# Performance work log

Measured on AMD Instinct MI355X. Metric: run time of the kernel, lower is better.

## Reference

```python
import jax, jax.numpy as jnp
import numpy as np

HOP = jnp.array([0, 1, 4, 7, 2, 5, 8, 3, 6, 9, 11, 14, 10, 12, 15, 13, 16])
GRAPH = jnp.array([0, 1, 4, 7, 2, 5, 8, 3, 6, 9, 12, 10, 13, 15, 11, 14, 16])
D_MODEL, L, D_INNER, D_STATE, DT_RANK = 512, 17, 1024, 4, 32


def layernorm(x, w, b, eps=1e-5):
    mu = x.mean(-1, keepdims=True)
    var = ((x - mu) ** 2).mean(-1, keepdims=True)
    return (x - mu) * jax.lax.rsqrt(var + eps) * w + b


def setup_inputs() -> dict:
    key = jax.random.key(0)
    ks = jax.random.split(key, 9)
    B = 4096
    s = lambda k, shape: jax.random.normal(k, shape, jnp.float32) * 0.02
    # A_log init per mamba_ssm: log(1..d_state) repeated over d_inner
    A_log = jnp.log(jnp.broadcast_to(jnp.arange(1, D_STATE + 1, dtype=jnp.float32), (D_INNER, D_STATE)))
    return {
        "x": jax.random.normal(ks[0], (B, L, D_MODEL), jnp.float32),
        "bp_embed": s(ks[1], (1, 5, D_MODEL)),
        "ln_w": jnp.ones((D_MODEL,), jnp.float32),
        "ln_b": jnp.zeros((D_MODEL,), jnp.float32),
        "in_proj_w": s(ks[2], (2 * D_INNER, D_MODEL)),
        "conv_w": 1.0 + s(ks[3], (D_INNER,)),  # d_conv=1 depthwise conv == per-channel scale
        "conv_b": jnp.zeros((D_INNER,), jnp.float32),
        "x_proj_w": s(ks[4], (DT_RANK + 2 * D_STATE, D_INNER)),
        "dt_proj_w": s(ks[5], (D_INNER, DT_RANK)),
        "dt_proj_b": s(ks[6], (D_INNER,)) - 4.0,  # softplus-inverse-ish small dt init
        "A_log": A_log,
        "D": jnp.ones((D_INNER,), jnp.float32),
        "out_proj_w": s(ks[7], (D_MODEL, D_INNER)),
    }


def mamba(u, in_proj_w, conv_w, conv_b, x_proj_w, dt_proj_w, dt_proj_b, A_log, D, out_proj_w):
    # u: [B, L, d_model]
    xz = jnp.einsum('bld,ed->ble', u, in_proj_w)          # [B,L,2*d_inner]
    xm, z = jnp.split(xz, 2, axis=-1)
    xm = jax.nn.silu(xm * conv_w + conv_b)                 # d_conv=1 -> pointwise
    x_dbl = jnp.einsum('ble,fe->blf', xm, x_proj_w)        # [B,L,dt_rank+2*d_state]
    dt_r = x_dbl[..., :DT_RANK]
    Bm = x_dbl[..., DT_RANK:DT_RANK + D_STATE]
    Cm = x_dbl[..., DT_RANK + D_STATE:]
    dt = jax.nn.softplus(jnp.einsum('blr,er->ble', dt_r, dt_proj_w) + dt_proj_b)  # [B,L,d_inner]
    A = -jnp.exp(A_log)                                    # [d_inner,d_state]

    def step(h, inp):
        dt_t, B_t, C_t, x_t = inp                          # [B,di],[B,ds],[B,ds],[B,di]
        dA = jnp.exp(dt_t[..., None] * A)                  # [B,di,ds]
        h = dA * h + (dt_t * x_t)[..., None] * B_t[:, None, :]
        y = jnp.einsum('bes,bs->be', h, C_t)
        return h, y

    bsz = u.shape[0]
    h0 = jnp.zeros((bsz, D_INNER, D_STATE), u.dtype)
    seq = (dt.transpose(1, 0, 2), Bm.transpose(1, 0, 2), Cm.transpose(1, 0, 2), xm.transpose(1, 0, 2))
    _, ys = jax.lax.scan(step, h0, seq)                    # ys: [L,B,d_inner]
    y = ys.transpose(1, 0, 2) + xm * D
    y = y * jax.nn.silu(z)
    return jnp.einsum('ble,de->bld', y, out_proj_w)


def reference(x, bp_embed, ln_w, ln_b, in_proj_w, conv_w, conv_b, x_proj_w,
              dt_proj_w, dt_proj_b, A_log, D, out_proj_w):
    bp = bp_embed
    x_bpe = jnp.concatenate([bp[:, :3], bp[:, :3], bp[:, :3], bp[:, :1],
                             bp[:, 3:], bp[:, :1], bp[:, 3:], bp[:, 3:]], axis=1)  # [1,17,dim]
    x_ssm = x[:, HOP, :] + x_bpe
    x_ssm = layernorm(x_ssm, ln_w, ln_b)
    x_ssm = mamba(x_ssm, in_proj_w, conv_w, conv_b, x_proj_w,
                  dt_proj_w, dt_proj_b, A_log, D, out_proj_w)
    return x + x_ssm[:, GRAPH, :]
```

## Files before the change

kernel.cpp:

```cpp
#include <hip/hip_runtime.h>

typedef unsigned short u16;
typedef unsigned int   u32;
typedef __bf16 bf16_t;
typedef bf16_t bf16x8 __attribute__((ext_vector_type(8)));
typedef float  f32x4  __attribute__((ext_vector_type(4)));

#define DEV static __device__ __forceinline__

__constant__ int c_HOP[17] = {0,1,4,7,2,5,8,3,6,9,11,14,10,12,15,13,16};
__constant__ int c_BPE[17] = {0,1,2,0,1,2,0,1,2,0,3,4,0,3,4,3,4};

DEV u16 f2bf(float f){
  u32 x = __builtin_bit_cast(u32, f);
  x += 0x7fffu + ((x >> 16) & 1u);
  return (u16)(x >> 16);
}
DEV float bf2f(u32 u){ return __builtin_bit_cast(float, u << 16); }
DEV float silu_f(float v){ return v / (1.f + __expf(-v)); }
DEV float softplus_f(float s){ return (s > 20.f) ? s : log1pf(__expf(s)); }

DEV void gll16(const void* g, void* l){
  __builtin_amdgcn_global_load_lds((__attribute__((address_space(1))) void*)g,
                                   (__attribute__((address_space(3))) void*)l,
                                   16, 0, 0);
}

__global__ __launch_bounds__(256) void cvt4(
    const float* __restrict__ s0, u16* __restrict__ d0, int n0,
    const float* __restrict__ s1, u16* __restrict__ d1, int n1,
    const float* __restrict__ s2, u16* __restrict__ d2, int n2,
    const float* __restrict__ s3, u16* __restrict__ d3, int n3)
{
  int t = blockIdx.x * 256 + threadIdx.x;
  if (t < n0){ d0[t] = f2bf(s0[t]); return; }
  t -= n0; if (t < n1){ d1[t] = f2bf(s1[t]); return; }
  t -= n1; if (t < n2){ d2[t] = f2bf(s2[t]); return; }
  t -= n2; if (t < n3){ d3[t] = f2bf(s3[t]); }
}

__global__ __launch_bounds__(256) void ln_gather(
    const float* __restrict__ x, const float* __restrict__ bpe,
    const float* __restrict__ lnw, const float* __restrict__ lnb,
    u16* __restrict__ u)
{
  int tok = blockIdx.x;
  int b = tok / 17;
  int l = tok - b * 17;
  const float* xr = x   + ((size_t)b * 17 + c_HOP[l]) * 512;
  const float* br = bpe + (size_t)c_BPE[l] * 512;
  int tid = threadIdx.x;
  int d0 = tid * 2;
  float2 xv = *(const float2*)(xr + d0);
  float2 bv = *(const float2*)(br + d0);
  float v0 = xv.x + bv.x, v1 = xv.y + bv.y;

  __shared__ float red[8];
  float s = v0 + v1;
  #pragma unroll
  for (int o = 32; o; o >>= 1) s += __shfl_xor(s, o);
  if ((tid & 63) == 0) red[tid >> 6] = s;
  __syncthreads();
  float mu = (red[0] + red[1] + red[2] + red[3]) * (1.f / 512.f);
  float a0 = v0 - mu, a1 = v1 - mu;
  float q = a0 * a0 + a1 * a1;
  #pragma unroll
  for (int o = 32; o; o >>= 1) q += __shfl_xor(q, o);
  if ((tid & 63) == 0) red[4 + (tid >> 6)] = q;
  __syncthreads();
  float var = (red[4] + red[5] + red[6] + red[7]) * (1.f / 512.f);
  float rs = rsqrtf(var + 1e-5f);

  u16 o0 = f2bf(a0 * rs * lnw[d0]     + lnb[d0]);
  u16 o1 = f2bf(a1 * rs * lnw[d0 + 1] + lnb[d0 + 1]);
  u32 pack = (u32)o0 | ((u32)o1 << 16);
  *(u32*)(u + (size_t)tok * 512 + d0) = pack;
}

enum { EPI_SPLIT = 0, EPI_OUT = 1 };

template<int EPI>
__global__ __launch_bounds__(512, 2) void gemm256(
    const u16* __restrict__ A, int lda,
    const u16* __restrict__ W, int K, int MT,
    u16* __restrict__ ob0, u16* __restrict__ ob1,
    const float* __restrict__ p0, const float* __restrict__ p1,
    const float* __restrict__ xres, float* __restrict__ fout)
{
  __shared__ u16 smem[65536];

  int nwg = gridDim.x;
  int cpx = nwg >> 3;
  int wg = (blockIdx.x & 7) * cpx + (blockIdx.x >> 3);
  int NT = nwg / MT;
  int nt = wg % NT, mt = wg / NT;
  int brow = mt * 256, bcol = nt * 256;
  int tid = threadIdx.x, lane = tid & 63, wid = tid >> 6;
  int wm = wid >> 2, wn = wid & 3;
  int l15 = lane & 15, lhi = lane >> 4;

  f32x4 acc[8][4] = {};

  int sr0 = tid >> 2, sr1 = 128 + (tid >> 2), sch = tid & 3;
  const u16* gA0 = A + (size_t)(brow + sr0) * lda + (sch ^ ((sr0 >> 1) & 3)) * 8;
  const u16* gA1 = A + (size_t)(brow + sr1) * lda + (sch ^ ((sr1 >> 1) & 3)) * 8;
  const u16* gW0 = W + (size_t)(bcol + sr0) * K   + (sch ^ ((sr0 >> 1) & 3)) * 8;
  const u16* gW1 = W + (size_t)(bcol + sr1) * K   + (sch ^ ((sr1 >> 1) & 3)) * 8;

  auto stA = [&](int buf, int kh, int koff) {
    char* d = (char*)smem + (buf * 2 + kh) * 16384 + tid * 16;
    gll16(gA0 + koff, d);
    gll16(gA1 + koff, d + 8192);
  };
  auto stB = [&](int buf, int kh, int koff) {
    char* d = (char*)smem + 65536 + (buf * 2 + kh) * 16384 + tid * 16;
    gll16(gW0 + koff, d);
    gll16(gW1 + koff, d + 8192);
  };

  int aoff[2][4], boff[4];
  #pragma unroll
  for (int mh = 0; mh < 2; mh++)
    #pragma unroll
    for (int mi = 0; mi < 4; mi++) {
      int r = wm * 128 + mh * 64 + mi * 16 + l15;
      aoff[mh][mi] = r * 64 + ((lhi ^ ((r >> 1) & 3)) * 16);
    }
  #pragma unroll
  for (int ni = 0; ni < 4; ni++) {
    int r = wn * 64 + ni * 16 + l15;
    boff[ni] = r * 64 + ((lhi ^ ((r >> 1) & 3)) * 16);
  }

#define HALF(BUF, KH)                                                        \
  {                                                                          \
    const char* la = (const char*)smem + ((BUF) * 2 + (KH)) * 16384;         \
    const char* lb = (const char*)smem + 65536 + ((BUF) * 2 + (KH)) * 16384; \
    bf16x8 bv0 = *(const bf16x8*)(lb + boff[0]);                             \
    bf16x8 bv1 = *(const bf16x8*)(lb + boff[1]);                             \
    bf16x8 bv2 = *(const bf16x8*)(lb + boff[2]);                             \
    bf16x8 bv3 = *(const bf16x8*)(lb + boff[3]);                             \
    bf16x8 a0 = *(const bf16x8*)(la + aoff[0][0]);                           \
    bf16x8 a1 = *(const bf16x8*)(la + aoff[0][1]);                           \
    bf16x8 a2 = *(const bf16x8*)(la + aoff[0][2]);                           \
    bf16x8 a3 = *(const bf16x8*)(la + aoff[0][3]);                           \
    __builtin_amdgcn_s_setprio(1);                                           \
    acc[0][0] = __builtin_amdgcn_mfma_f32_16x16x32_bf16(a0, bv0, acc[0][0],0,0,0); \
    acc[1][0] = __builtin_amdgcn_mfma_f32_16x16x32_bf16(a1, bv0, acc[1][0],0,0,0); \
    acc[2][0] = __builtin_amdgcn_mfma_f32_16x16x32_bf16(a2, bv0, acc[2][0],0,0,0); \
    acc[3][0] = __builtin_amdgcn_mfma_f32_16x16x32_bf16(a3, bv0, acc[3][0],0,0,0); \
    acc[0][1] = __builtin_amdgcn_mfma_f32_16x16x32_bf16(a0, bv1, acc[0][1],0,0,0); \
    acc[1][1] = __builtin_amdgcn_mfma_f32_16x16x32_bf16(a1, bv1, acc[1][1],0,0,0); \
    acc[2][1] = __builtin_amdgcn_mfma_f32_16x16x32_bf16(a2, bv1, acc[2][1],0,0,0); \
    acc[3][1] = __builtin_amdgcn_mfma_f32_16x16x32_bf16(a3, bv1, acc[3][1],0,0,0); \
    acc[0][2] = __builtin_amdgcn_mfma_f32_16x16x32_bf16(a0, bv2, acc[0][2],0,0,0); \
    acc[1][2] = __builtin_amdgcn_mfma_f32_16x16x32_bf16(a1, bv2, acc[1][2],0,0,0); \
    acc[2][2] = __builtin_amdgcn_mfma_f32_16x16x32_bf16(a2, bv2, acc[2][2],0,0,0); \
    acc[3][2] = __builtin_amdgcn_mfma_f32_16x16x32_bf16(a3, bv2, acc[3][2],0,0,0); \
    acc[0][3] = __builtin_amdgcn_mfma_f32_16x16x32_bf16(a0, bv3, acc[0][3],0,0,0); \
    acc[1][3] = __builtin_amdgcn_mfma_f32_16x16x32_bf16(a1, bv3, acc[1][3],0,0,0); \
    acc[2][3] = __builtin_amdgcn_mfma_f32_16x16x32_bf16(a2, bv3, acc[2][3],0,0,0); \
    acc[3][3] = __builtin_amdgcn_mfma_f32_16x16x32_bf16(a3, bv3, acc[3][3],0,0,0); \
    a0 = *(const bf16x8*)(la + aoff[1][0]);                                  \
    a1 = *(const bf16x8*)(la + aoff[1][1]);                                  \
    a2 = *(const bf16x8*)(la + aoff[1][2]);                                  \
    a3 = *(const bf16x8*)(la + aoff[1][3]);                                  \
    acc[4][0] = __builtin_amdgcn_mfma_f32_16x16x32_bf16(a0, bv0, acc[4][0],0,0,0); \
    acc[5][0] = __builtin_amdgcn_mfma_f32_16x16x32_bf16(a1, bv0, acc[5][0],0,0,0); \
    acc[6][0] = __builtin_amdgcn_mfma_f32_16x16x32_bf16(a2, bv0, acc[6][0],0,0,0); \
    acc[7][0] = __builtin_amdgcn_mfma_f32_16x16x32_bf16(a3, bv0, acc[7][0],0,0,0); \
    acc[4][1] = __builtin_amdgcn_mfma_f32_16x16x32_bf16(a0, bv1, acc[4][1],0,0,0); \
    acc[5][1] = __builtin_amdgcn_mfma_f32_16x16x32_bf16(a1, bv1, acc[5][1],0,0,0); \
    acc[6][1] = __builtin_amdgcn_mfma_f32_16x16x32_bf16(a2, bv1, acc[6][1],0,0,0); \
    acc[7][1] = __builtin_amdgcn_mfma_f32_16x16x32_bf16(a3, bv1, acc[7][1],0,0,0); \
    acc[4][2] = __builtin_amdgcn_mfma_f32_16x16x32_bf16(a0, bv2, acc[4][2],0,0,0); \
    acc[5][2] = __builtin_amdgcn_mfma_f32_16x16x32_bf16(a1, bv2, acc[5][2],0,0,0); \
    acc[6][2] = __builtin_amdgcn_mfma_f32_16x16x32_bf16(a2, bv2, acc[6][2],0,0,0); \
    acc[7][2] = __builtin_amdgcn_mfma_f32_16x16x32_bf16(a3, bv2, acc[7][2],0,0,0); \
    acc[4][3] = __builtin_amdgcn_mfma_f32_16x16x32_bf16(a0, bv3, acc[4][3],0,0,0); \
    acc[5][3] = __builtin_amdgcn_mfma_f32_16x16x32_bf16(a1, bv3, acc[5][3],0,0,0); \
    acc[6][3] = __builtin_amdgcn_mfma_f32_16x16x32_bf16(a2, bv3, acc[6][3],0,0,0); \
    acc[7][3] = __builtin_amdgcn_mfma_f32_16x16x32_bf16(a3, bv3, acc[7][3],0,0,0); \
    __builtin_amdgcn_s_setprio(0);                                           \
  }

  int T = K >> 6;

  stA(0, 0, 0);  stB(0, 0, 0);
  stA(0, 1, 32); stB(0, 1, 32);
  stA(1, 0, 64); stB(1, 0, 64);
  asm volatile("s_waitcnt vmcnt(8)" ::: "memory");
  __builtin_amdgcn_s_barrier();
  __builtin_amdgcn_sched_barrier(0);

  for (int t = 0; t < T; ++t) {
    int bb_ = t & 1;
    if (t + 1 < T) { int ko = ((t + 1) << 6) + 32; stA(bb_ ^ 1, 1, ko); stB(bb_ ^ 1, 1, ko); }
    HALF(bb_, 0);
    if (t < T - 1) { asm volatile("s_waitcnt vmcnt(8)" ::: "memory"); }
    else           { asm volatile("s_waitcnt vmcnt(0)" ::: "memory"); }
    __builtin_amdgcn_s_barrier();
    __builtin_amdgcn_sched_barrier(0);
    if (t + 2 < T) { int ko = (t + 2) << 6; stA(bb_, 0, ko); stB(bb_, 0, ko); }
    HALF(bb_, 1);
    if (t < T - 2)      { asm volatile("s_waitcnt vmcnt(8)" ::: "memory"); }
    else if (t == T - 2){ asm volatile("s_waitcnt vmcnt(4)" ::: "memory"); }
    else                { asm volatile("s_waitcnt vmcnt(0)" ::: "memory"); }
    __builtin_amdgcn_s_barrier();
    __builtin_amdgcn_sched_barrier(0);
  }
#undef HALF

  if constexpr (EPI == EPI_SPLIT) {
    u16* cl = smem;
    bool isx = (bcol < 1024);
    #pragma unroll
    for (int fm = 0; fm < 8; fm++) {
      int lrow = wm * 128 + fm * 16 + lhi * 4;
      #pragma unroll
      for (int ni = 0; ni < 4; ni++) {
        int col = wn * 64 + ni * 16 + l15;
        int cidx = isx ? (bcol + col) : 0;
        float cw = isx ? p0[cidx] : 1.f;
        float cb = isx ? p1[cidx] : 0.f;
        #pragma unroll
        for (int rr = 0; rr < 4; rr++)
          cl[(lrow + rr) * 256 + col] = f2bf(silu_f(acc[fm][ni][rr] * cw + cb));
      }
    }
    __syncthreads();
    int colbase = isx ? bcol : (bcol - 1024);
    u16* dst = isx ? ob0 : ob1;
    #pragma unroll
    for (int i = 0; i < 16; i++) {
      int idx = i * 512 + tid;
      int row = idx >> 5;
      int q = idx & 31;
      uint4 v = *(const uint4*)(cl + row * 256 + q * 8);
      *(uint4*)(dst + (size_t)(brow + row) * 1024 + colbase + q * 8) = v;
    }
  } else {
    float* cf = (float*)smem;
    #pragma unroll
    for (int mh = 0; mh < 2; mh++) {
      __syncthreads();
      if (wm == mh) {
        #pragma unroll
        for (int fm = 0; fm < 8; fm++) {
          int lrow = fm * 16 + lhi * 4;
          #pragma unroll
          for (int ni = 0; ni < 4; ni++) {
            int col = wn * 64 + ni * 16 + l15;
            #pragma unroll
            for (int rr = 0; rr < 4; rr++)
              cf[(lrow + rr) * 256 + col] = acc[fm][ni][rr];
          }
        }
      }
      __syncthreads();
      #pragma unroll
      for (int i = 0; i < 16; i++) {
        int idx = i * 512 + tid;
        int row = idx >> 6;
        int q = idx & 63;
        int grow = brow + mh * 128 + row;
        u32 bq = (u32)grow / 17u;
        int gl = grow - (int)bq * 17;
        size_t orow = (size_t)bq * 17 + c_HOP[gl];
        size_t off = orow * 512 + bcol + q * 4;
        float4 xv = *(const float4*)(xres + off);
        const float* cp = cf + row * 256 + q * 4;
        float4 ov;
        ov.x = xv.x + cp[0]; ov.y = xv.y + cp[1];
        ov.z = xv.z + cp[2]; ov.w = xv.w + cp[3];
        *(float4*)(fout + off) = ov;
      }
    }
  }
}

enum { EPI_XDBL = 0, EPI_DT = 1 };

template<int EPI>
__global__ __launch_bounds__(256) void gemm_bt(
    const u16* __restrict__ A, int lda,
    const u16* __restrict__ W, int K, int MT,
    u16* __restrict__ ob0, const float* __restrict__ p0)
{
  __shared__ u16 sm[16384];
  int nwg = gridDim.x;
  int cpx = nwg >> 3;
  int wg = (blockIdx.x & 7) * cpx + (blockIdx.x >> 3);
  int NT = nwg / MT;
  int nt = wg % NT, mt = wg / NT;
  int brow = mt * 128, bcol = nt * 128;
  int tid = threadIdx.x, lane = tid & 63, wid = tid >> 6;
  int wm = wid >> 1, wn = wid & 1;

  f32x4 acc[4][4] = {};

  int srow = tid >> 2;
  int sch  = tid & 3;

  const u16* gA0 = A + (size_t)(brow + srow)      * lda + (sch ^ ((srow >> 1) & 3)) * 8;
  const u16* gA1 = A + (size_t)(brow + 64 + srow) * lda + (sch ^ (((64 + srow) >> 1) & 3)) * 8;
  const u16* gW0 = W + (size_t)(bcol + srow)      * K   + (sch ^ ((srow >> 1) & 3)) * 8;
  const u16* gW1 = W + (size_t)(bcol + 64 + srow) * K   + (sch ^ (((64 + srow) >> 1) & 3)) * 8;

  auto STAGE = [&](int buf, int kt) {
    char* dA = (char*)sm + buf * 8192 + tid * 16;
    char* dW = (char*)sm + 16384 + buf * 8192 + tid * 16;
    gll16(gA0 + kt, dA);
    gll16(gA1 + kt, dA + 4096);
    gll16(gW0 + kt, dW);
    gll16(gW1 + kt, dW + 4096);
  };

  int aoff[4], boff[4];
  #pragma unroll
  for (int mi = 0; mi < 4; mi++) {
    int r = wm * 64 + mi * 16 + (lane & 15);
    aoff[mi] = r * 64 + (((lane >> 4) ^ ((r >> 1) & 3)) * 16);
  }
  #pragma unroll
  for (int ni = 0; ni < 4; ni++) {
    int r = wn * 64 + ni * 16 + (lane & 15);
    boff[ni] = r * 64 + (((lane >> 4) ^ ((r >> 1) & 3)) * 16);
  }

  auto COMPUTE = [&](int buf) {
    const char* la = (const char*)sm + buf * 8192;
    const char* lb = (const char*)sm + 16384 + buf * 8192;
    bf16x8 av[4], bv[4];
    #pragma unroll
    for (int mi = 0; mi < 4; mi++)
      av[mi] = *(const bf16x8*)(la + aoff[mi]);
    #pragma unroll
    for (int ni = 0; ni < 4; ni++)
      bv[ni] = *(const bf16x8*)(lb + boff[ni]);
    #pragma unroll
    for (int mi = 0; mi < 4; mi++)
      #pragma unroll
      for (int ni = 0; ni < 4; ni++)
        acc[mi][ni] = __builtin_amdgcn_mfma_f32_16x16x32_bf16(
            av[mi], bv[ni], acc[mi][ni], 0, 0, 0);
  };

  int nsteps = K >> 5;
  STAGE(0, 0);
  __syncthreads();
  int cur = 0;
  for (int s = 1; s < nsteps; ++s) {
    STAGE(cur ^ 1, s << 5);
    COMPUTE(cur);
    __syncthreads();
    cur ^= 1;
  }
  COMPUTE(cur);

  int r4 = (lane >> 4) * 4;
  int cl15 = lane & 15;
  if constexpr (EPI == EPI_XDBL) {
    #pragma unroll
    for (int mi = 0; mi < 4; mi++) {
      int rowb = brow + wm * 64 + mi * 16 + r4;
      #pragma unroll
      for (int ni = 0; ni < 4; ni++) {
        int col = bcol + wn * 64 + ni * 16 + cl15;
        if (col < 40) {
          #pragma unroll
          for (int rr = 0; rr < 4; rr++)
            ob0[(size_t)(rowb + rr) * 40 + col] = f2bf(acc[mi][ni][rr]);
        }
      }
    }
  } else {
    __syncthreads();
    u16* cls = sm;
    #pragma unroll
    for (int mi = 0; mi < 4; mi++) {
      int lrow = wm * 64 + mi * 16 + r4;
      #pragma unroll
      for (int ni = 0; ni < 4; ni++) {
        int lcol = wn * 64 + ni * 16 + cl15;
        float bb = p0[bcol + lcol];
        #pragma unroll
        for (int rr = 0; rr < 4; rr++)
          cls[(lrow + rr) * 128 + lcol] = f2bf(softplus_f(acc[mi][ni][rr] + bb));
      }
    }
    __syncthreads();
    #pragma unroll
    for (int i = 0; i < 8; i++) {
      int idx = i * 256 + tid;
      int row = idx >> 4;
      int q = idx & 15;
      uint4 v = *(const uint4*)(cls + row * 128 + q * 8);
      *(uint4*)(ob0 + (size_t)(brow + row) * 1024 + bcol + q * 8) = v;
    }
  }
}

__global__ __launch_bounds__(128) void scan5(
    const u16* __restrict__ xm, const u16* __restrict__ zs,
    const u16* __restrict__ xdbl, u16* __restrict__ dty,
    const float* __restrict__ A_log, const float* __restrict__ Dp)
{
  int b = blockIdx.x;
  int tid = threadIdx.x;
  int e0 = tid * 8;
  const size_t base = (size_t)b * 17 * 1024;

  float4 al = *(const float4*)(A_log + (size_t)e0 * 4);
  float A0 = -__expf(al.x), A1 = -__expf(al.y);
  float A2 = -__expf(al.z), A3 = -__expf(al.w);
  float Dv[8];
  *(float4*)(Dv)     = *(const float4*)(Dp + e0);
  *(float4*)(Dv + 4) = *(const float4*)(Dp + e0 + 4);

  const u16* xmb = xm + base + e0;
  const u16* zsb = zs + base + e0;
  u16* db = dty + base + e0;
  const u16* bcb = xdbl + (size_t)b * 680 + 32;

  float h[8][4];
  #pragma unroll
  for (int c = 0; c < 8; c++)
    #pragma unroll
    for (int s = 0; s < 4; s++) h[c][s] = 0.f;

  #pragma unroll
  for (int t = 0; t < 17; t++) {
    uint4 xr = *(const uint4*)(xmb + t * 1024);
    uint4 zr = *(const uint4*)(zsb + t * 1024);
    uint4 dr = *(const uint4*)(db + t * 1024);
    uint4 bc = *(const uint4*)(bcb + t * 40);
    float B0 = bf2f(bc.x & 0xffffu), B1 = bf2f(bc.x >> 16);
    float B2 = bf2f(bc.y & 0xffffu), B3 = bf2f(bc.y >> 16);
    float C0 = bf2f(bc.z & 0xffffu), C1 = bf2f(bc.z >> 16);
    float C2 = bf2f(bc.w & 0xffffu), C3 = bf2f(bc.w >> 16);
    u32 yo[4];
    const u32* xw = (const u32*)&xr;
    const u32* zw = (const u32*)&zr;
    const u32* dw = (const u32*)&dr;
    #pragma unroll
    for (int c = 0; c < 8; c++) {
      u32 x16 = (c & 1) ? (xw[c >> 1] >> 16) : (xw[c >> 1] & 0xffffu);
      u32 z16 = (c & 1) ? (zw[c >> 1] >> 16) : (zw[c >> 1] & 0xffffu);
      u32 d16 = (c & 1) ? (dw[c >> 1] >> 16) : (dw[c >> 1] & 0xffffu);
      float xv = bf2f(x16), zv = bf2f(z16), dtv = bf2f(d16);
      float dx = dtv * xv;
      h[c][0] = __expf(dtv * A0) * h[c][0] + dx * B0;
      h[c][1] = __expf(dtv * A1) * h[c][1] + dx * B1;
      h[c][2] = __expf(dtv * A2) * h[c][2] + dx * B2;
      h[c][3] = __expf(dtv * A3) * h[c][3] + dx * B3;
      float yv = h[c][0] * C0 + h[c][1] * C1 + h[c][2] * C2 + h[c][3] * C3;
      u16 pk = f2bf((yv + xv * Dv[c]) * zv);
      if (c & 1) yo[c >> 1] |= ((u32)pk << 16);
      else       yo[c >> 1] = (u32)pk;
    }
    *(uint4*)(db + t * 1024) = *(uint4*)yo;
  }
}

extern "C" void kernel_launch(void* const* d_in, const int* in_sizes, int n_in,
                              void* d_out, int out_size, void* d_ws, size_t ws_size,
                              hipStream_t stream) {
  const float* x     = (const float*)d_in[0];
  const float* bpe   = (const float*)d_in[1];
  const float* lnw   = (const float*)d_in[2];
  const float* lnb   = (const float*)d_in[3];
  const float* w_in  = (const float*)d_in[4];
  const float* convw = (const float*)d_in[5];
  const float* convb = (const float*)d_in[6];
  const float* w_xp  = (const float*)d_in[7];
  const float* w_dt  = (const float*)d_in[8];
  const float* b_dt  = (const float*)d_in[9];
  const float* A_log = (const float*)d_in[10];
  const float* Dp    = (const float*)d_in[11];
  const float* w_out = (const float*)d_in[12];
  float* out = (float*)d_out;

  u16* ws = (u16*)d_ws;
  u16* wb_in  = ws;
  u16* wb_out = wb_in  + 1048576;
  u16* wb_xp  = wb_out + 524288;
  u16* wb_dt  = wb_xp  + 40960;
  u16* xm     = wb_dt  + 32768;
  u16* zs     = xm     + 71303168;
  u16* xdbl   = zs     + 71303168;
  u16* dty    = xdbl   + 2785280;
  u16* u      = dty;

  const int MT2 = 272;
  const int MT1 = 544;

  cvt4<<<6432, 256, 0, stream>>>(w_in, wb_in, 1048576, w_out, wb_out, 524288,
                                 w_xp, wb_xp, 40960, w_dt, wb_dt, 32768);

  ln_gather<<<69632, 256, 0, stream>>>(x, bpe, lnw, lnb, u);

  gemm256<EPI_SPLIT><<<MT2 * 8, 512, 0, stream>>>(
      u, 512, wb_in, 512, MT2, xm, zs, convw, convb, nullptr, nullptr);

  gemm_bt<EPI_XDBL><<<MT1 * 1, 256, 0, stream>>>(
      xm, 1024, wb_xp, 1024, MT1, xdbl, nullptr);

  gemm_bt<EPI_DT><<<MT1 * 8, 256, 0, stream>>>(
      xdbl, 40, wb_dt, 32, MT1, dty, b_dt);

  scan5<<<4096, 128, 0, stream>>>(xm, zs, xdbl, dty, A_log, Dp);

  gemm256<EPI_OUT><<<MT2 * 2, 512, 0, stream>>>(
      dty, 1024, wb_out, 1024, MT2, nullptr, nullptr, nullptr, nullptr, x, out);
}
```

Baseline: 842.3 us.

## Reschedule GEMM main loop into four barrier phases and swizzle epilogue LDS staging

The big GEMM main loop is split into four phases per K-step, each loading A fragments and issuing the next tile's global-to-LDS loads for one operand before a barrier and MFMA cluster. The prefetch depth drops from two half-tiles ahead to one full tile ahead, with a single vmcnt wait every two phases. Separately, the epilogue LDS staging buffers in the fused-GEMM and dt GEMM kernels are written and read with a row-dependent rotated column index to avoid bank conflicts. The extra barriers add synchronisation cost, and the shallower prefetch may expose more global-load latency.

```diff
diff --git a/kernel.cpp b/kernel.cpp
--- a/kernel.cpp
+++ b/kernel.cpp
@@ -132,84 +132,77 @@
     boff[ni] = r * 64 + ((lhi ^ ((r >> 1) & 3)) * 16);
   }
 
-#define HALF(BUF, KH)                                                        \
-  {                                                                          \
-    const char* la = (const char*)smem + ((BUF) * 2 + (KH)) * 16384;         \
-    const char* lb = (const char*)smem + 65536 + ((BUF) * 2 + (KH)) * 16384; \
-    bf16x8 bv0 = *(const bf16x8*)(lb + boff[0]);                             \
-    bf16x8 bv1 = *(const bf16x8*)(lb + boff[1]);                             \
-    bf16x8 bv2 = *(const bf16x8*)(lb + boff[2]);                             \
-    bf16x8 bv3 = *(const bf16x8*)(lb + boff[3]);                             \
-    bf16x8 a0 = *(const bf16x8*)(la + aoff[0][0]);                           \
-    bf16x8 a1 = *(const bf16x8*)(la + aoff[0][1]);                           \
-    bf16x8 a2 = *(const bf16x8*)(la + aoff[0][2]);                           \
-    bf16x8 a3 = *(const bf16x8*)(la + aoff[0][3]);                           \
-    __builtin_amdgcn_s_setprio(1);                                           \
-    acc[0][0] = __builtin_amdgcn_mfma_f32_16x16x32_bf16(a0, bv0, acc[0][0],0,0,0); \
-    acc[1][0] = __builtin_amdgcn_mfma_f32_16x16x32_bf16(a1, bv0, acc[1][0],0,0,0); \
-    acc[2][0] = __builtin_amdgcn_mfma_f32_16x16x32_bf16(a2, bv0, acc[2][0],0,0,0); \
-    acc[3][0] = __builtin_amdgcn_mfma_f32_16x16x32_bf16(a3, bv0, acc[3][0],0,0,0); \
-    acc[0][1] = __builtin_amdgcn_mfma_f32_16x16x32_bf16(a0, bv1, acc[0][1],0,0,0); \
-    acc[1][1] = __builtin_amdgcn_mfma_f32_16x16x32_bf16(a1, bv1, acc[1][1],0,0,0); \
-    acc[2][1] = __builtin_amdgcn_mfma_f32_16x16x32_bf16(a2, bv1, acc[2][1],0,0,0); \
-    acc[3][1] = __builtin_amdgcn_mfma_f32_16x16x32_bf16(a3, bv1, acc[3][1],0,0,0); \
-    acc[0][2] = __builtin_amdgcn_mfma_f32_16x16x32_bf16(a0, bv2, acc[0][2],0,0,0); \
-    acc[1][2] = __builtin_amdgcn_mfma_f32_16x16x32_bf16(a1, bv2, acc[1][2],0,0,0); \
-    acc[2][2] = __builtin_amdgcn_mfma_f32_16x16x32_bf16(a2, bv2, acc[2][2],0,0,0); \
-    acc[3][2] = __builtin_amdgcn_mfma_f32_16x16x32_bf16(a3, bv2, acc[3][2],0,0,0); \
-    acc[0][3] = __builtin_amdgcn_mfma_f32_16x16x32_bf16(a0, bv3, acc[0][3],0,0,0); \
-    acc[1][3] = __builtin_amdgcn_mfma_f32_16x16x32_bf16(a1, bv3, acc[1][3],0,0,0); \
-    acc[2][3] = __builtin_amdgcn_mfma_f32_16x16x32_bf16(a2, bv3, acc[2][3],0,0,0); \
-    acc[3][3] = __builtin_amdgcn_mfma_f32_16x16x32_bf16(a3, bv3, acc[3][3],0,0,0); \
-    a0 = *(const bf16x8*)(la + aoff[1][0]);                                  \
-    a1 = *(const bf16x8*)(la + aoff[1][1]);                                  \
-    a2 = *(const bf16x8*)(la + aoff[1][2]);                                  \
-    a3 = *(const bf16x8*)(la + aoff[1][3]);                                  \
-    acc[4][0] = __builtin_amdgcn_mfma_f32_16x16x32_bf16(a0, bv0, acc[4][0],0,0,0); \
-    acc[5][0] = __builtin_amdgcn_mfma_f32_16x16x32_bf16(a1, bv0, acc[5][0],0,0,0); \
-    acc[6][0] = __builtin_amdgcn_mfma_f32_16x16x32_bf16(a2, bv0, acc[6][0],0,0,0); \
-    acc[7][0] = __builtin_amdgcn_mfma_f32_16x16x32_bf16(a3, bv0, acc[7][0],0,0,0); \
-    acc[4][1] = __builtin_amdgcn_mfma_f32_16x16x32_bf16(a0, bv1, acc[4][1],0,0,0); \
-    acc[5][1] = __builtin_amdgcn_mfma_f32_16x16x32_bf16(a1, bv1, acc[5][1],0,0,0); \
-    acc[6][1] = __builtin_amdgcn_mfma_f32_16x16x32_bf16(a2, bv1, acc[6][1],0,0,0); \
-    acc[7][1] = __builtin_amdgcn_mfma_f32_16x16x32_bf16(a3, bv1, acc[7][1],0,0,0); \
-    acc[4][2] = __builtin_amdgcn_mfma_f32_16x16x32_bf16(a0, bv2, acc[4][2],0,0,0); \
-    acc[5][2] = __builtin_amdgcn_mfma_f32_16x16x32_bf16(a1, bv2, acc[5][2],0,0,0); \
-    acc[6][2] = __builtin_amdgcn_mfma_f32_16x16x32_bf16(a2, bv2, acc[6][2],0,0,0); \
-    acc[7][2] = __builtin_amdgcn_mfma_f32_16x16x32_bf16(a3, bv2, acc[7][2],0,0,0); \
-    acc[4][3] = __builtin_amdgcn_mfma_f32_16x16x32_bf16(a0, bv3, acc[4][3],0,0,0); \
-    acc[5][3] = __builtin_amdgcn_mfma_f32_16x16x32_bf16(a1, bv3, acc[5][3],0,0,0); \
-    acc[6][3] = __builtin_amdgcn_mfma_f32_16x16x32_bf16(a2, bv3, acc[6][3],0,0,0); \
-    acc[7][3] = __builtin_amdgcn_mfma_f32_16x16x32_bf16(a3, bv3, acc[7][3],0,0,0); \
-    __builtin_amdgcn_s_setprio(0);                                           \
+  bf16x8 bvv[4];
+
+#define PH(BUF, KH, MH, LOADB, STMT, WAIT)                                  \
+  {                                                                         \
+    const char* la = (const char*)smem + ((BUF) * 2 + (KH)) * 16384;        \
+    bf16x8 a0 = *(const bf16x8*)(la + aoff[MH][0]);                         \
+    bf16x8 a1 = *(const bf16x8*)(la + aoff[MH][1]);                         \
+    bf16x8 a2 = *(const bf16x8*)(la + aoff[MH][2]);                         \
+    bf16x8 a3 = *(const bf16x8*)(la + aoff[MH][3]);                         \
+    if (LOADB) {                                                            \
+      const char* lb = (const char*)smem + 65536 + ((BUF) * 2 + (KH)) * 16384; \
+      bvv[0] = *(const bf16x8*)(lb + boff[0]);                              \
+      bvv[1] = *(const bf16x8*)(lb + boff[1]);                              \
+      bvv[2] = *(const bf16x8*)(lb + boff[2]);                              \
+      bvv[3] = *(const bf16x8*)(lb + boff[3]);                              \
+    }                                                                       \
+    STMT                                                                    \
+    __builtin_amdgcn_sched_barrier(0);                                      \
+    __builtin_amdgcn_s_barrier();                                           \
+    __builtin_amdgcn_s_setprio(1);                                          \
+    acc[(MH)*4+0][0] = __builtin_amdgcn_mfma_f32_16x16x32_bf16(a0, bvv[0], acc[(MH)*4+0][0],0,0,0); \
+    acc[(MH)*4+1][0] = __builtin_amdgcn_mfma_f32_16x16x32_bf16(a1, bvv[0], acc[(MH)*4+1][0],0,0,0); \
+    acc[(MH)*4+2][0] = __builtin_amdgcn_mfma_f32_16x16x32_bf16(a2, bvv[0], acc[(MH)*4+2][0],0,0,0); \
+    acc[(MH)*4+3][0] = __builtin_amdgcn_mfma_f32_16x16x32_bf16(a3, bvv[0], acc[(MH)*4+3][0],0,0,0); \
+    acc[(MH)*4+0][1] = __builtin_amdgcn_mfma_f32_16x16x32_bf16(a0, bvv[1], acc[(MH)*4+0][1],0,0,0); \
+    acc[(MH)*4+1][1] = __builtin_amdgcn_mfma_f32_16x16x32_bf16(a1, bvv[1], acc[(MH)*4+1][1],0,0,0); \
+    acc[(MH)*4+2][1] = __builtin_amdgcn_mfma_f32_16x16x32_bf16(a2, bvv[1], acc[(MH)*4+2][1],0,0,0); \
+    acc[(MH)*4+3][1] = __builtin_amdgcn_mfma_f32_16x16x32_bf16(a3, bvv[1], acc[(MH)*4+3][1],0,0,0); \
+    acc[(MH)*4+0][2] = __builtin_amdgcn_mfma_f32_16x16x32_bf16(a0, bvv[2], acc[(MH)*4+0][2],0,0,0); \
+    acc[(MH)*4+1][2] = __builtin_amdgcn_mfma_f32_16x16x32_bf16(a1, bvv[2], acc[(MH)*4+1][2],0,0,0); \
+    acc[(MH)*4+2][2] = __builtin_amdgcn_mfma_f32_16x16x32_bf16(a2, bvv[2], acc[(MH)*4+2][2],0,0,0); \
+    acc[(MH)*4+3][2] = __builtin_amdgcn_mfma_f32_16x16x32_bf16(a3, bvv[2], acc[(MH)*4+3][2],0,0,0); \
+    acc[(MH)*4+0][3] = __builtin_amdgcn_mfma_f32_16x16x32_bf16(a0, bvv[3], acc[(MH)*4+0][3],0,0,0); \
+    acc[(MH)*4+1][3] = __builtin_amdgcn_mfma_f32_16x16x32_bf16(a1, bvv[3], acc[(MH)*4+1][3],0,0,0); \
+    acc[(MH)*4+2][3] = __builtin_amdgcn_mfma_f32_16x16x32_bf16(a2, bvv[3], acc[(MH)*4+2][3],0,0,0); \
+    acc[(MH)*4+3][3] = __builtin_amdgcn_mfma_f32_16x16x32_bf16(a3, bvv[3], acc[(MH)*4+3][3],0,0,0); \
+    __builtin_amdgcn_s_setprio(0);                                          \
+    WAIT                                                                    \
+    __builtin_amdgcn_s_barrier();                                           \
+    __builtin_amdgcn_sched_barrier(0);                                      \
   }
 
   int T = K >> 6;
 
   stA(0, 0, 0);  stB(0, 0, 0);
   stA(0, 1, 32); stB(0, 1, 32);
-  stA(1, 0, 64); stB(1, 0, 64);
-  asm volatile("s_waitcnt vmcnt(8)" ::: "memory");
+  asm volatile("s_waitcnt vmcnt(4)" ::: "memory");
   __builtin_amdgcn_s_barrier();
   __builtin_amdgcn_sched_barrier(0);
 
   for (int t = 0; t < T; ++t) {
-    int bb_ = t & 1;
-    if (t + 1 < T) { int ko = ((t + 1) << 6) + 32; stA(bb_ ^ 1, 1, ko); stB(bb_ ^ 1, 1, ko); }
-    HALF(bb_, 0);
-    if (t < T - 1) { asm volatile("s_waitcnt vmcnt(8)" ::: "memory"); }
-    else           { asm volatile("s_waitcnt vmcnt(0)" ::: "memory"); }
-    __builtin_amdgcn_s_barrier();
-    __builtin_amdgcn_sched_barrier(0);
-    if (t + 2 < T) { int ko = (t + 2) << 6; stA(bb_, 0, ko); stB(bb_, 0, ko); }
-    HALF(bb_, 1);
-    if (t < T - 2)      { asm volatile("s_waitcnt vmcnt(8)" ::: "memory"); }
-    else if (t == T - 2){ asm volatile("s_waitcnt vmcnt(4)" ::: "memory"); }
-    else                { asm volatile("s_waitcnt vmcnt(0)" ::: "memory"); }
-    __builtin_amdgcn_s_barrier();
-    __builtin_amdgcn_sched_barrier(0);
-  }
-#undef HALF
+    int bf = t & 1, nb = bf ^ 1;
+    int nk = (t + 1) << 6;
+    bool s = (t + 1 < T);
+    PH(bf, 0, 0, true,  { if (s) stA(nb, 0, nk); }, {});
+    if (s) {
+      PH(bf, 0, 1, false, { stB(nb, 0, nk); },
+         { asm volatile("s_waitcnt vmcnt(4)" ::: "memory"); });
+    } else {
+      PH(bf, 0, 1, false, {},
+         { asm volatile("s_waitcnt vmcnt(0)" ::: "memory"); });
+    }
+    PH(bf, 1, 0, true,  { if (s) stA(nb, 1, nk + 32); }, {});
+    if (s) {
+      PH(bf, 1, 1, false, { stB(nb, 1, nk + 32); },
+         { asm volatile("s_waitcnt vmcnt(4)" ::: "memory"); });
+    } else {
+      PH(bf, 1, 1, false, {}, {});
+    }
+  }
+#undef PH
 
   if constexpr (EPI == EPI_SPLIT) {
     u16* cl = smem;
@@ -224,8 +217,11 @@
         float cw = isx ? p0[cidx] : 1.f;
         float cb = isx ? p1[cidx] : 0.f;
         #pragma unroll
-        for (int rr = 0; rr < 4; rr++)
-          cl[(lrow + rr) * 256 + col] = f2bf(silu_f(acc[fm][ni][rr] * cw + cb));
+        for (int rr = 0; rr < 4; rr++) {
+          int row = lrow + rr;
+          cl[row * 256 + ((col + row * 8) & 255)] =
+              f2bf(silu_f(acc[fm][ni][rr] * cw + cb));
+        }
       }
     }
     __syncthreads();
@@ -236,7 +232,7 @@
       int idx = i * 512 + tid;
       int row = idx >> 5;
       int q = idx & 31;
-      uint4 v = *(const uint4*)(cl + row * 256 + q * 8);
+      uint4 v = *(const uint4*)(cl + row * 256 + ((q * 8 + row * 8) & 255));
       *(uint4*)(dst + (size_t)(brow + row) * 1024 + colbase + q * 8) = v;
     }
   } else {
@@ -252,8 +248,10 @@
           for (int ni = 0; ni < 4; ni++) {
             int col = wn * 64 + ni * 16 + l15;
             #pragma unroll
-            for (int rr = 0; rr < 4; rr++)
-              cf[(lrow + rr) * 256 + col] = acc[fm][ni][rr];
+            for (int rr = 0; rr < 4; rr++) {
+              int row = lrow + rr;
+              cf[row * 256 + ((col + row * 4) & 255)] = acc[fm][ni][rr];
+            }
           }
         }
       }
@@ -269,7 +267,7 @@
         size_t orow = (size_t)bq * 17 + c_HOP[gl];
         size_t off = orow * 512 + bcol + q * 4;
         float4 xv = *(const float4*)(xres + off);
-        const float* cp = cf + row * 256 + q * 4;
+        const float* cp = cf + row * 256 + ((q * 4 + row * 4) & 255);
         float4 ov;
         ov.x = xv.x + cp[0]; ov.y = xv.y + cp[1];
         ov.z = xv.z + cp[2]; ov.w = xv.w + cp[3];
@@ -385,8 +383,11 @@
         int lcol = wn * 64 + ni * 16 + cl15;
         float bb = p0[bcol + lcol];
         #pragma unroll
-        for (int rr = 0; rr < 4; rr++)
-          cls[(lrow + rr) * 128 + lcol] = f2bf(softplus_f(acc[mi][ni][rr] + bb));
+        for (int rr = 0; rr < 4; rr++) {
+          int row = lrow + rr;
+          cls[row * 128 + ((lcol + row * 8) & 127)] =
+              f2bf(softplus_f(acc[mi][ni][rr] + bb));
+        }
       }
     }
     __syncthreads();
@@ -395,7 +396,7 @@
       int idx = i * 256 + tid;
       int row = idx >> 4;
       int q = idx & 15;
-      uint4 v = *(const uint4*)(cls + row * 128 + q * 8);
+      uint4 v = *(const uint4*)(cls + row * 128 + ((q * 8 + row * 8) & 127));
       *(uint4*)(ob0 + (size_t)(brow + row) * 1024 + bcol + q * 8) = v;
     }
   }
```

After: 846.3 us. About the same (+0.5%).

## Replace out-projection 256x256 GEMM with 128x128 tile kernel reading weights from global

Applied to the files above, without the earlier changes.

Replaces the out-projection GEMM with a dedicated kernel. It uses 128x128 tiles, 256 threads and 4 blocks per CU, which yields 2176 workgroups instead of 544. Only the A operand is staged in LDS, double-buffered. The weight B fragments are loaded straight from global/L2 into registers. The epilogue now adds the residual and scatters directly from registers instead of going through an LDS transpose. This is meant to improve occupancy and load balance for the N=512 output GEMM, at the cost of uncoalesced scalar epilogue stores and less reuse per tile.

```diff
diff --git a/kernel.cpp b/kernel.cpp
--- a/kernel.cpp
+++ b/kernel.cpp
@@ -77,15 +77,14 @@
   *(u32*)(u + (size_t)tok * 512 + d0) = pack;
 }
 
-enum { EPI_SPLIT = 0, EPI_OUT = 1 };
+enum { EPI_SPLIT = 0 };
 
 template<int EPI>
 __global__ __launch_bounds__(512, 2) void gemm256(
     const u16* __restrict__ A, int lda,
     const u16* __restrict__ W, int K, int MT,
     u16* __restrict__ ob0, u16* __restrict__ ob1,
-    const float* __restrict__ p0, const float* __restrict__ p1,
-    const float* __restrict__ xres, float* __restrict__ fout)
+    const float* __restrict__ p0, const float* __restrict__ p1)
 {
   __shared__ u16 smem[65536];
 
@@ -211,7 +210,7 @@
   }
 #undef HALF
 
-  if constexpr (EPI == EPI_SPLIT) {
+  {
     u16* cl = smem;
     bool isx = (bcol < 1024);
     #pragma unroll
@@ -239,41 +238,99 @@
       uint4 v = *(const uint4*)(cl + row * 256 + q * 8);
       *(uint4*)(dst + (size_t)(brow + row) * 1024 + colbase + q * 8) = v;
     }
-  } else {
-    float* cf = (float*)smem;
-    #pragma unroll
-    for (int mh = 0; mh < 2; mh++) {
-      __syncthreads();
-      if (wm == mh) {
-        #pragma unroll
-        for (int fm = 0; fm < 8; fm++) {
-          int lrow = fm * 16 + lhi * 4;
-          #pragma unroll
-          for (int ni = 0; ni < 4; ni++) {
-            int col = wn * 64 + ni * 16 + l15;
-            #pragma unroll
-            for (int rr = 0; rr < 4; rr++)
-              cf[(lrow + rr) * 256 + col] = acc[fm][ni][rr];
-          }
-        }
-      }
-      __syncthreads();
+  }
+}
+
+__global__ __launch_bounds__(256, 4) void gemm_oc(
+    const u16* __restrict__ A,
+    const u16* __restrict__ W,
+    const float* __restrict__ xres, float* __restrict__ fout)
+{
+  __shared__ u16 sA[2][4096];
+
+  int nwg = gridDim.x;
+  int cpx = nwg >> 3;
+  int wg = (blockIdx.x & 7) * cpx + (blockIdx.x >> 3);
+  int nt = wg & 3, mt = wg >> 2;
+  int brow = mt * 128, bcol = nt * 128;
+  int tid = threadIdx.x, lane = tid & 63, wid = tid >> 6;
+  int wm = wid >> 1, wn = wid & 1;
+  int l15 = lane & 15, lhi = lane >> 4;
+
+  f32x4 acc[4][4] = {};
+
+  int srow = tid >> 2, sch = tid & 3;
+  const u16* gA0 = A + (size_t)(brow + srow)      * 1024 + (sch ^ ((srow >> 1) & 3)) * 8;
+  const u16* gA1 = A + (size_t)(brow + 64 + srow) * 1024 + (sch ^ (((64 + srow) >> 1) & 3)) * 8;
+
+  auto STAGE = [&](int buf, int kt) {
+    char* d = (char*)sA[buf] + tid * 16;
+    gll16(gA0 + kt, d);
+    gll16(gA1 + kt, d + 4096);
+  };
+
+  int aoff[4];
+  #pragma unroll
+  for (int mi = 0; mi < 4; mi++) {
+    int r = wm * 64 + mi * 16 + l15;
+    aoff[mi] = r * 64 + ((lhi ^ ((r >> 1) & 3)) * 16);
+  }
+  const u16* wp[4];
+  #pragma unroll
+  for (int ni = 0; ni < 4; ni++)
+    wp[ni] = W + (size_t)(bcol + wn * 64 + ni * 16 + l15) * 1024 + lhi * 8;
+
+  const int T = 32;
+  STAGE(0, 0);
+  __syncthreads();
+  for (int t = 0; t < T; ++t) {
+    if (t + 1 < T) STAGE((t + 1) & 1, (t + 1) << 5);
+    int kk = t << 5;
+    bf16x8 bv0 = *(const bf16x8*)(wp[0] + kk);
+    bf16x8 bv1 = *(const bf16x8*)(wp[1] + kk);
+    bf16x8 bv2 = *(const bf16x8*)(wp[2] + kk);
+    bf16x8 bv3 = *(const bf16x8*)(wp[3] + kk);
+    const char* la = (const char*)sA[t & 1];
+    bf16x8 a0 = *(const bf16x8*)(la + aoff[0]);
+    bf16x8 a1 = *(const bf16x8*)(la + aoff[1]);
+    bf16x8 a2 = *(const bf16x8*)(la + aoff[2]);
+    bf16x8 a3 = *(const bf16x8*)(la + aoff[3]);
+    __builtin_amdgcn_s_setprio(1);
+    acc[0][0] = __builtin_amdgcn_mfma_f32_16x16x32_bf16(a0, bv0, acc[0][0],0,0,0);
+    acc[1][0] = __builtin_amdgcn_mfma_f32_16x16x32_bf16(a1, bv0, acc[1][0],0,0,0);
+    acc[2][0] = __builtin_amdgcn_mfma_f32_16x16x32_bf16(a2, bv0, acc[2][0],0,0,0);
+    acc[3][0] = __builtin_amdgcn_mfma_f32_16x16x32_bf16(a3, bv0, acc[3][0],0,0,0);
+    acc[0][1] = __builtin_amdgcn_mfma_f32_16x16x32_bf16(a0, bv1, acc[0][1],0,0,0);
+    acc[1][1] = __builtin_amdgcn_mfma_f32_16x16x32_bf16(a1, bv1, acc[1][1],0,0,0);
+    acc[2][1] = __builtin_amdgcn_mfma_f32_16x16x32_bf16(a2, bv1, acc[2][1],0,0,0);
+    acc[3][1] = __builtin_amdgcn_mfma_f32_16x16x32_bf16(a3, bv1, acc[3][1],0,0,0);
+    acc[0][2] = __builtin_amdgcn_mfma_f32_16x16x32_bf16(a0, bv2, acc[0][2],0,0,0);
+    acc[1][2] = __builtin_amdgcn_mfma_f32_16x16x32_bf16(a1, bv2, acc[1][2],0,0,0);
+    acc[2][2] = __builtin_amdgcn_mfma_f32_16x16x32_bf16(a2, bv2, acc[2][2],0,0,0);
+    acc[3][2] = __builtin_amdgcn_mfma_f32_16x16x32_bf16(a3, bv2, acc[3][2],0,0,0);
+    acc[0][3] = __builtin_amdgcn_mfma_f32_16x16x32_bf16(a0, bv3, acc[0][3],0,0,0);
+    acc[1][3] = __builtin_amdgcn_mfma_f32_16x16x32_bf16(a1, bv3, acc[1][3],0,0,0);
+    acc[2][3] = __builtin_amdgcn_mfma_f32_16x16x32_bf16(a2, bv3, acc[2][3],0,0,0);
+    acc[3][3] = __builtin_amdgcn_mfma_f32_16x16x32_bf16(a3, bv3, acc[3][3],0,0,0);
+    __builtin_amdgcn_s_setprio(0);
+    __syncthreads();
+  }
+
+  int r4 = lhi * 4;
+  #pragma unroll
+  for (int mi = 0; mi < 4; mi++) {
+    int rowb = brow + wm * 64 + mi * 16 + r4;
+    #pragma unroll
+    for (int rr = 0; rr < 4; rr++) {
+      int row = rowb + rr;
+      u32 bq = (u32)row / 17u;
+      int gl = row - (int)bq * 17;
+      size_t orow = ((size_t)bq * 17 + c_HOP[gl]) * 512;
       #pragma unroll
-      for (int i = 0; i < 16; i++) {
-        int idx = i * 512 + tid;
-        int row = idx >> 6;
-        int q = idx & 63;
-        int grow = brow + mh * 128 + row;
-        u32 bq = (u32)grow / 17u;
-        int gl = grow - (int)bq * 17;
-        size_t orow = (size_t)bq * 17 + c_HOP[gl];
-        size_t off = orow * 512 + bcol + q * 4;
-        float4 xv = *(const float4*)(xres + off);
-        const float* cp = cf + row * 256 + q * 4;
-        float4 ov;
-        ov.x = xv.x + cp[0]; ov.y = xv.y + cp[1];
-        ov.z = xv.z + cp[2]; ov.w = xv.w + cp[3];
-        *(float4*)(fout + off) = ov;
+      for (int ni = 0; ni < 4; ni++) {
+        int col = bcol + wn * 64 + ni * 16 + l15;
+        size_t oi = orow + col;
+        fout[oi] = xres[oi] + acc[mi][ni][rr];
       }
     }
   }
@@ -501,7 +558,7 @@
   ln_gather<<<69632, 256, 0, stream>>>(x, bpe, lnw, lnb, u);
 
   gemm256<EPI_SPLIT><<<MT2 * 8, 512, 0, stream>>>(
-      u, 512, wb_in, 512, MT2, xm, zs, convw, convb, nullptr, nullptr);
+      u, 512, wb_in, 512, MT2, xm, zs, convw, convb);
 
   gemm_bt<EPI_XDBL><<<MT1 * 1, 256, 0, stream>>>(
       xm, 1024, wb_xp, 1024, MT1, xdbl, nullptr);
@@ -511,6 +568,5 @@
 
   scan5<<<4096, 128, 0, stream>>>(xm, zs, xdbl, dty, A_log, Dp);
 
-  gemm256<EPI_OUT><<<MT2 * 2, 512, 0, stream>>>(
-      dty, 1024, wb_out, 1024, MT2, nullptr, nullptr, nullptr, nullptr, x, out);
-}
+  gemm_oc<<<MT1 * 4, 256, 0, stream>>>(dty, wb_out, x, out);
+}
```

New measurement: 888.7 us. 1.06x slower.
